# Kernel tuning notes

Hardware: AMD Instinct MI355X
Metric: run time of the kernel (lower is better)

The kernel has to match this reference:

```python
import jax, jax.numpy as jnp
import numpy as np

B, S, D = 2, 2048, 1024
H = 16
HD = D // H  # 64
EPS = 1e-5
ROPE_BASE = 10000.0


def _rope_cos_sin(seq_len, head_dim, dtype):
    # inv_freq over even channel indices, standard rotate-half RoPE
    inv_freq = 1.0 / (ROPE_BASE ** (jnp.arange(0, head_dim, 2, dtype=jnp.float32) / head_dim))
    ang = jnp.arange(seq_len, dtype=jnp.float32)[:, None] * inv_freq[None, :]  # [S, HD/2]
    emb = jnp.concatenate([ang, ang], axis=-1)  # [S, HD]
    return jnp.cos(emb).astype(dtype), jnp.sin(emb).astype(dtype)


def _rotate_half(x):
    x1, x2 = jnp.split(x, 2, axis=-1)
    return jnp.concatenate([-x2, x1], axis=-1)


def setup_inputs() -> dict:
    key = jax.random.key(0)
    ks = jax.random.split(key, 5)
    std = 0.023  # default init_method: normal(mean=0, std=0.023)
    return {
        "hidden_states": jax.random.normal(ks[0], (B, S, D), dtype=jnp.float32),
        "ln_gamma": jnp.ones((D,), dtype=jnp.float32),
        "ln_beta": jnp.zeros((D,), dtype=jnp.float32),
        "qkv_weight": jax.random.normal(ks[1], (3 * D, D), dtype=jnp.float32) * std,
        "qkv_bias": jax.random.normal(ks[2], (3 * D,), dtype=jnp.float32) * std,
        "proj_weight": jax.random.normal(ks[3], (D, D), dtype=jnp.float32) * std,
        "proj_bias": jax.random.normal(ks[4], (D,), dtype=jnp.float32) * std,
    }


def reference(hidden_states, ln_gamma, ln_beta, qkv_weight, qkv_bias, proj_weight, proj_bias):
    b, s, d = hidden_states.shape
    # --- input LayerNorm ---
    mu = jnp.mean(hidden_states, axis=-1, keepdims=True)
    var = jnp.mean(jnp.square(hidden_states - mu), axis=-1, keepdims=True)
    x = (hidden_states - mu) * jax.lax.rsqrt(var + EPS) * ln_gamma + ln_beta

    # --- fused QKV projection (interleaved per-head q,k,v) ---
    qkv = x @ qkv_weight.T + qkv_bias  # [B,S,3D]
    qkv = qkv.reshape(b, s, H, 3, HD)
    q, k, v = qkv[..., 0, :], qkv[..., 1, :], qkv[..., 2, :]  # each [B,S,H,HD]

    # --- RoPE on q and k ---
    cos, sin = _rope_cos_sin(s, HD, q.dtype)  # [S,HD]
    cos = cos[None, :, None, :]
    sin = sin[None, :, None, :]
    q = q * cos + _rotate_half(q) * sin
    k = k * cos + _rotate_half(k) * sin

    # --- causal scaled-dot-product attention ---
    scale = 1.0 / jnp.sqrt(jnp.asarray(HD, dtype=q.dtype))
    scores = jnp.einsum("bqhd,bkhd->bhqk", q, k) * scale  # [B,H,S,S]
    causal = jnp.tril(jnp.ones((s, s), dtype=bool))
    scores = jnp.where(causal[None, None, :, :], scores, jnp.finfo(scores.dtype).min)
    probs = jax.nn.softmax(scores, axis=-1)
    ctx = jnp.einsum("bhqk,bkhd->bqhd", probs, v).reshape(b, s, d)

    # --- output projection ---
    return ctx @ proj_weight.T + proj_bias
```

## Files before the change

kernel.cpp:

```cpp
#include <hip/hip_runtime.h>
#include <math.h>

#define B_  2
#define S_  2048
#define D_  1024
#define H_  16
#define HD_ 64
#define BS_ (B_ * S_)

typedef __bf16 bf16_t;
typedef __bf16 bf16x8 __attribute__((ext_vector_type(8)));
typedef __bf16 bf16x4 __attribute__((ext_vector_type(4)));
typedef float  f32x4  __attribute__((ext_vector_type(4)));
typedef short  s16x4  __attribute__((ext_vector_type(4)));

#define QSCALE 0.18033688011112042f
#define FREQC  0.28782313662425575f

__device__ __forceinline__ void async_ld16(const bf16_t* g, bf16_t* l)
{
    __builtin_amdgcn_global_load_lds(
        (const __attribute__((address_space(1))) void*)g,
        (__attribute__((address_space(3))) void*)l,
        16, 0, 0);
}

__device__ __forceinline__ int chunk_base(int t)
{
    if (t < 8)  return t;
    if (t < 16) return 8 + 2 * (t - 8);
    if (t < 24) return 24 + 3 * (t - 16);
    return 48 + 4 * (t - 24);
}

__global__ __launch_bounds__(256) void ln_cvt(const float* __restrict__ x,
                                              const float* __restrict__ gamma,
                                              const float* __restrict__ beta,
                                              bf16_t* __restrict__ y,
                                              const float* __restrict__ wa,
                                              const float* __restrict__ wb,
                                              bf16_t* __restrict__ oa,
                                              bf16_t* __restrict__ ob)
{
    if (blockIdx.x >= BS_) {
        int idx = (blockIdx.x - BS_) * 256 + threadIdx.x;
        const int NA = 3 * D_ * D_ / 4;
        if (idx < NA) {
            float4 v = ((const float4*)wa)[idx];
            bf16x4 p;
            p[0] = (bf16_t)v.x; p[1] = (bf16_t)v.y; p[2] = (bf16_t)v.z; p[3] = (bf16_t)v.w;
            ((bf16x4*)oa)[idx] = p;
        } else {
            int j = idx - NA;
            float4 v = ((const float4*)wb)[j];
            bf16x4 p;
            p[0] = (bf16_t)v.x; p[1] = (bf16_t)v.y; p[2] = (bf16_t)v.z; p[3] = (bf16_t)v.w;
            ((bf16x4*)ob)[j] = p;
        }
        return;
    }
    int row = blockIdx.x;
    float4 v = ((const float4*)(x + (size_t)row * D_))[threadIdx.x];
    float sum = v.x + v.y + v.z + v.w;
    float sq  = v.x * v.x + v.y * v.y + v.z * v.z + v.w * v.w;
#pragma unroll
    for (int off = 32; off > 0; off >>= 1) {
        sum += __shfl_down(sum, off);
        sq  += __shfl_down(sq, off);
    }
    __shared__ float s_sum[4], s_sq[4];
    int wave = threadIdx.x >> 6;
    if ((threadIdx.x & 63) == 0) { s_sum[wave] = sum; s_sq[wave] = sq; }
    __syncthreads();
    float tsum = s_sum[0] + s_sum[1] + s_sum[2] + s_sum[3];
    float tsq  = s_sq[0] + s_sq[1] + s_sq[2] + s_sq[3];
    float mean = tsum * (1.0f / D_);
    float var  = tsq * (1.0f / D_) - mean * mean;
    float rstd = rsqrtf(var + 1e-5f);
    float4 g = ((const float4*)gamma)[threadIdx.x];
    float4 b = ((const float4*)beta)[threadIdx.x];
    bf16x4 o;
    o[0] = (bf16_t)((v.x - mean) * rstd * g.x + b.x);
    o[1] = (bf16_t)((v.y - mean) * rstd * g.y + b.y);
    o[2] = (bf16_t)((v.z - mean) * rstd * g.z + b.z);
    o[3] = (bf16_t)((v.w - mean) * rstd * g.w + b.w);
    *(bf16x4*)&y[(size_t)row * D_ + threadIdx.x * 4] = o;
}

template<int MODE, int TM>
__global__ __launch_bounds__(256) void gemm_bf16(const bf16_t* __restrict__ A,
                                                 const bf16_t* __restrict__ W,
                                                 const float* __restrict__ bias,
                                                 float* __restrict__ outf,
                                                 bf16_t* __restrict__ qout,
                                                 bf16_t* __restrict__ kout,
                                                 bf16_t* __restrict__ vout,
                                                 int M, int N, int K)
{
    constexpr int ASZ = TM * 32;
    constexpr int BUF = ASZ + 4096;
    constexpr int SMEM = (MODE == 1) ? 18432 : 2 * BUF;
    constexpr int MI = (TM == 128) ? 4 : 2;
    __shared__ bf16_t smem[SMEM];
    const int bm = blockIdx.y * TM, bn = blockIdx.x * 128;
    const int tid = threadIdx.x;
    const int wave = tid >> 6, lane = tid & 63;
    const int ln16 = lane & 15, quad = lane >> 4;
    const int wr = (wave >> 1) * (TM / 2), wc = (wave & 1) * 64;
    const int slot_a = (quad ^ (ln16 & 3)) * 8;

    f32x4 acc[MI][4];
#pragma unroll
    for (int i = 0; i < MI; i++)
#pragma unroll
        for (int j = 0; j < 4; j++) acc[i][j] = (f32x4){0.f, 0.f, 0.f, 0.f};

#pragma unroll
    for (int j = 0; j < TM / 64; j++) {
        int e = j * 256 + tid;
        int r = e >> 2, cg = ((e & 3) ^ (r & 3)) * 8;
        async_ld16(&A[(size_t)(bm + r) * K + cg], smem + e * 8);
    }
#pragma unroll
    for (int j = 0; j < 2; j++) {
        int e = j * 256 + tid;
        int r = e >> 2, cg = ((e & 3) ^ (r & 3)) * 8;
        async_ld16(&W[(size_t)(bn + r) * K + cg], smem + ASZ + e * 8);
    }
    __syncthreads();

    for (int k0 = 0, it = 0; k0 < K; k0 += 32, it++) {
        const bf16_t* cur = smem + (it & 1) * BUF;
        bf16_t* nxt = smem + ((it & 1) ^ 1) * BUF;
        if (k0 + 32 < K) {
#pragma unroll
            for (int j = 0; j < TM / 64; j++) {
                int e = j * 256 + tid;
                int r = e >> 2, cg = ((e & 3) ^ (r & 3)) * 8;
                async_ld16(&A[(size_t)(bm + r) * K + k0 + 32 + cg], nxt + e * 8);
            }
#pragma unroll
            for (int j = 0; j < 2; j++) {
                int e = j * 256 + tid;
                int r = e >> 2, cg = ((e & 3) ^ (r & 3)) * 8;
                async_ld16(&W[(size_t)(bn + r) * K + k0 + 32 + cg], nxt + ASZ + e * 8);
            }
        }

        bf16x8 af[MI], bf[4];
#pragma unroll
        for (int mi = 0; mi < MI; mi++)
            af[mi] = *(const bf16x8*)&cur[(wr + mi * 16 + ln16) * 32 + slot_a];
#pragma unroll
        for (int ni = 0; ni < 4; ni++)
            bf[ni] = *(const bf16x8*)&cur[ASZ + (wc + ni * 16 + ln16) * 32 + slot_a];
#pragma unroll
        for (int mi = 0; mi < MI; mi++)
#pragma unroll
            for (int ni = 0; ni < 4; ni++)
                acc[mi][ni] = __builtin_amdgcn_mfma_f32_16x16x32_bf16(
                    af[mi], bf[ni], acc[mi][ni], 0, 0, 0);

        __syncthreads();
    }

#pragma unroll
    for (int ni = 0; ni < 4; ni++) {
        float bb = bias[bn + wc + ni * 16 + ln16];
#pragma unroll
        for (int mi = 0; mi < MI; mi++)
#pragma unroll
            for (int r = 0; r < 4; r++) acc[mi][ni][r] += bb;
    }

    if (MODE == 0) {
#pragma unroll
        for (int ni = 0; ni < 4; ni++) {
            int n = bn + wc + ni * 16 + ln16;
#pragma unroll
            for (int mi = 0; mi < MI; mi++)
#pragma unroll
                for (int r = 0; r < 4; r++)
                    outf[(size_t)(bm + wr + mi * 16 + quad * 4 + r) * N + n] = acc[mi][ni][r];
        }
    } else {
        const int n64 = (bn + wc) >> 6;
        const int t = n64 % 3, h = n64 / 3;
        bf16_t* T = smem + wave * (64 * 72);
        if (t == 2) {
#pragma unroll
            for (int mi = 0; mi < 4; mi++) {
#pragma unroll
                for (int ni = 0; ni < 4; ni++) {
                    bf16x4 pk;
#pragma unroll
                    for (int r = 0; r < 4; r++) pk[r] = (bf16_t)acc[mi][ni][r];
                    *(bf16x4*)&T[(ni * 16 + ln16) * 72 + mi * 16 + quad * 4] = pk;
                }
            }
            int m0 = bm + wr;
            int bi = m0 >> 11, s0g = m0 & (S_ - 1);
#pragma unroll
            for (int e = lane; e < 512; e += 64) {
                int hd_l = e >> 3, c8 = (e & 7) << 3;
                *(bf16x8*)&vout[((size_t)(bi * H_ + h) * HD_ + hd_l) * S_ + s0g + c8] =
                    *(const bf16x8*)&T[hd_l * 72 + c8];
            }
        } else {
            float fr0 = __expf(-(float)ln16 * FREQC);
            float fr1 = __expf(-(float)(16 + ln16) * FREQC);
            float sc = (t == 0) ? QSCALE : 1.0f;
#pragma unroll
            for (int mi = 0; mi < 4; mi++) {
#pragma unroll
                for (int r = 0; r < 4; r++) {
                    int m = bm + wr + mi * 16 + quad * 4 + r;
                    float s = (float)(m & (S_ - 1));
                    float sn0, cs0, sn1, cs1;
                    __sincosf(s * fr0, &sn0, &cs0);
                    __sincosf(s * fr1, &sn1, &cs1);
                    int rowo = (mi * 16 + quad * 4 + r) * 72;
                    float x1 = acc[mi][0][r], x2 = acc[mi][2][r];
                    T[rowo + ln16]      = (bf16_t)((x1 * cs0 - x2 * sn0) * sc);
                    T[rowo + 32 + ln16] = (bf16_t)((x2 * cs0 + x1 * sn0) * sc);
                    x1 = acc[mi][1][r]; x2 = acc[mi][3][r];
                    T[rowo + 16 + ln16] = (bf16_t)((x1 * cs1 - x2 * sn1) * sc);
                    T[rowo + 48 + ln16] = (bf16_t)((x2 * cs1 + x1 * sn1) * sc);
                }
            }
            bf16_t* dst = (t == 0) ? qout : kout;
#pragma unroll
            for (int e = lane; e < 512; e += 64) {
                int row_l = e >> 3, c8 = (e & 7) << 3;
                int m = bm + wr + row_l;
                int b = m >> 11, s = m & (S_ - 1);
                *(bf16x8*)&dst[((size_t)(b * H_ + h) * S_ + s) * HD_ + c8] =
                    *(const bf16x8*)&T[row_l * 72 + c8];
            }
        }
    }
}

__global__ __launch_bounds__(512) void attn_p1(const bf16_t* __restrict__ q_buf,
                                               const bf16_t* __restrict__ k_buf,
                                               const bf16_t* __restrict__ v_t,
                                               bf16_t* __restrict__ part_o,
                                               float* __restrict__ part_l)
{
    __shared__ bf16_t KS[2][4096];
    __shared__ bf16_t VS[2][4096];

    const int h = blockIdx.y, b = blockIdx.z;
    const int xx = 39 - blockIdx.x;
    int T, c;
    if (xx < 4)       { T = xx;                 c = 0; }
    else if (xx < 12) { int y = xx - 4;  T = 4 + (y >> 1); c = y & 1; }
    else if (xx < 24) { int y = xx - 12; int q = y / 3; T = 8 + q; c = y - 3 * q; }
    else              { int y = xx - 24; T = 12 + (y >> 2); c = y & 3; }
    const int k0c = c * 8;
    const int k1c = min(2 * T + 1, k0c + 7);

    const int tid = threadIdx.x;
    const int wave = tid >> 6, lane = tid & 63;
    const int ln16 = lane & 15, quad = lane >> 4;
    const int w0 = T * 128 + wave * 16;
    const int dt = w0 >> 6;
    const int s7 = ln16 & 7;

    const bf16_t* qb = q_buf + (size_t)(b * H_ + h) * S_ * HD_;
    const bf16_t* kb = k_buf + (size_t)(b * H_ + h) * S_ * HD_;
    const bf16_t* vb = v_t  + (size_t)(b * H_ + h) * HD_ * S_;

    const int r0 = tid >> 3, c0 = ((tid & 7) ^ (r0 & 7)) * 8;

    bf16x8 qf[2];
#pragma unroll
    for (int kc = 0; kc < 2; kc++)
        qf[kc] = *(const bf16x8*)&qb[(size_t)(w0 + ln16) * HD_ + kc * 32 + quad * 8];

    f32x4 o[4];
#pragma unroll
    for (int mi = 0; mi < 4; mi++) o[mi] = (f32x4){0.f, 0.f, 0.f, 0.f};
    float l_i = 0.f;

    async_ld16(&kb[(size_t)(k0c * 64 + r0) * HD_ + c0], &KS[0][tid * 8]);
    async_ld16(&vb[(size_t)r0 * S_ + k0c * 64 + c0], &VS[0][tid * 8]);
    __syncthreads();

    for (int kt = k0c; kt <= k1c; kt++) {
        const int cb = (kt - k0c) & 1;
        if (kt < k1c) {
            const int nb = cb ^ 1, kn = kt + 1;
            async_ld16(&kb[(size_t)(kn * 64 + r0) * HD_ + c0], &KS[nb][tid * 8]);
            async_ld16(&vb[(size_t)r0 * S_ + kn * 64 + c0], &VS[nb][tid * 8]);
        }

        const bf16_t* Kc = &KS[cb][0];
        const bf16_t* Vc = &VS[cb][0];

        f32x4 st[4];
#pragma unroll
        for (int cbx = 0; cbx < 4; cbx++) st[cbx] = (f32x4){0.f, 0.f, 0.f, 0.f};
#pragma unroll
        for (int kc = 0; kc < 2; kc++)
#pragma unroll
            for (int cbx = 0; cbx < 4; cbx++) {
                bf16x8 kf = *(const bf16x8*)&Kc[(cbx * 16 + ln16) * 64 + ((kc * 4 + quad) ^ s7) * 8];
                st[cbx] = __builtin_amdgcn_mfma_f32_16x16x32_bf16(kf, qf[kc], st[cbx], 0, 0, 0);
            }

        if (kt >= dt) {
            int q_g = w0 + ln16;
#pragma unroll
            for (int cbx = 0; cbx < 4; cbx++) {
                int key0 = kt * 64 + cbx * 16 + quad * 4;
#pragma unroll
                for (int r = 0; r < 4; r++)
                    if (key0 + r > q_g) st[cbx][r] = -1e30f;
            }
        }

#pragma unroll
        for (int cbx = 0; cbx < 4; cbx++)
#pragma unroll
            for (int r = 0; r < 4; r++) {
                float p = exp2f(st[cbx][r]);
                st[cbx][r] = p;
                l_i += p;
            }

        s16x4 pf4[4];
#pragma unroll
        for (int cbx = 0; cbx < 4; cbx++) {
            union { bf16x4 hv; s16x4 sv; } u;
#pragma unroll
            for (int r = 0; r < 4; r++) u.hv[r] = (bf16_t)st[cbx][r];
            pf4[cbx] = u.sv;
        }

#pragma unroll
        for (int cbx = 0; cbx < 4; cbx++) {
            int slot = ((cbx * 2 + (quad >> 1)) ^ s7) * 8 + (quad & 1) * 4;
#pragma unroll
            for (int mi = 0; mi < 4; mi++) {
                union { bf16x4 hv; s16x4 sv; } uv;
                uv.hv = *(const bf16x4*)&Vc[(mi * 16 + ln16) * 64 + slot];
                o[mi] = __builtin_amdgcn_mfma_f32_16x16x16bf16_1k(uv.sv, pf4[cbx], o[mi], 0, 0, 0);
            }
        }

        __syncthreads();
    }

    l_i += __shfl_xor(l_i, 16);
    l_i += __shfl_xor(l_i, 32);

    const int t_tile = dt;
    const size_t pidx = (size_t)(b * H_ + h) * 80 + chunk_base(t_tile) + c;
    bf16_t* po = part_o + pidx * 4096;
    const int q_l = (wave & 3) * 16 + ln16;
#pragma unroll
    for (int mi = 0; mi < 4; mi++) {
        bf16x4 pk;
#pragma unroll
        for (int r = 0; r < 4; r++) pk[r] = (bf16_t)o[mi][r];
        *(bf16x4*)&po[q_l * 64 + mi * 16 + quad * 4] = pk;
    }
    if (quad == 0)
        part_l[pidx * 64 + q_l] = l_i;
}

__global__ __launch_bounds__(256) void attn_p2(const bf16_t* __restrict__ part_o,
                                               const float* __restrict__ part_l,
                                               bf16_t* __restrict__ ctx)
{
    const int t = blockIdx.x, h = blockIdx.y, b = blockIdx.z;
    const int nch = (t >> 3) + 1;
    const size_t p0 = (size_t)(b * H_ + h) * 80 + chunk_base(t);
    const int q_l = threadIdx.x >> 2;
    const int hg = (threadIdx.x & 3) * 16;

    float L = 0.f;
    float f0[8] = {0,0,0,0,0,0,0,0}, f1[8] = {0,0,0,0,0,0,0,0};
#pragma unroll
    for (int i = 0; i < 4; i++) {
        if (i < nch) {
            L += part_l[(p0 + i) * 64 + q_l];
            const bf16_t* oi = part_o + (p0 + i) * 4096 + q_l * 64 + hg;
            bf16x8 v0 = *(const bf16x8*)oi;
            bf16x8 v1 = *(const bf16x8*)(oi + 8);
#pragma unroll
            for (int j = 0; j < 8; j++) {
                f0[j] += (float)v0[j];
                f1[j] += (float)v1[j];
            }
        }
    }
    float invL = 1.0f / L;
    bf16x8 out0, out1;
#pragma unroll
    for (int j = 0; j < 8; j++) {
        out0[j] = (bf16_t)(f0[j] * invL);
        out1[j] = (bf16_t)(f1[j] * invL);
    }
    bf16_t* dst = &ctx[(size_t)(b * S_ + t * 64 + q_l) * D_ + h * HD_ + hg];
    *(bf16x8*)dst = out0;
    *(bf16x8*)(dst + 8) = out1;
}

extern "C" void kernel_launch(void* const* d_in, const int* in_sizes, int n_in,
                              void* d_out, int out_size, void* d_ws, size_t ws_size,
                              hipStream_t stream)
{
    const float* hidden = (const float*)d_in[0];
    const float* gamma  = (const float*)d_in[1];
    const float* beta   = (const float*)d_in[2];
    const float* qkv_w  = (const float*)d_in[3];
    const float* qkv_b  = (const float*)d_in[4];
    const float* proj_w = (const float*)d_in[5];
    const float* proj_b = (const float*)d_in[6];
    float* out = (float*)d_out;

    char* ws = (char*)d_ws;
    const size_t MB = 1024 * 1024;
    bf16_t* x_ln = (bf16_t*)(ws);
    bf16_t* wq   = (bf16_t*)(ws +  8 * MB);
    bf16_t* wp   = (bf16_t*)(ws + 14 * MB);
    bf16_t* qbf  = (bf16_t*)(ws + 16 * MB);
    bf16_t* kbf  = (bf16_t*)(ws + 24 * MB);
    bf16_t* vtb  = (bf16_t*)(ws + 32 * MB);
    bf16_t* ctx  = (bf16_t*)(ws + 40 * MB);
    bf16_t* po   = (bf16_t*)(ws + 48 * MB);
    float*  pl   = (float*)(ws + 68 * MB);

    ln_cvt<<<BS_ + 4096, 256, 0, stream>>>(hidden, gamma, beta, x_ln,
                                           qkv_w, proj_w, wq, wp);
    gemm_bf16<1, 128><<<dim3(24, 32), 256, 0, stream>>>(
        x_ln, wq, qkv_b, nullptr, qbf, kbf, vtb, BS_, 3 * D_, D_);
    attn_p1<<<dim3(40, H_, B_), 512, 0, stream>>>(qbf, kbf, vtb, po, pl);
    attn_p2<<<dim3(32, H_, B_), 256, 0, stream>>>(po, pl, ctx);
    gemm_bf16<0, 64><<<dim3(8, 64), 256, 0, stream>>>(
        ctx, wp, proj_b, out, nullptr, nullptr, nullptr, BS_, D_, D_);
}
```

Baseline: 186.6 us.

## Skip fully-masked key tiles and compute row sums via MFMA with ones

Inside the attention loop, waves now skip QK/PV compute for key tiles beyond their diagonal tile, and masking runs only on the diagonal tile. The softmax denominator is now accumulated by an extra MFMA against a ones vector using the bf16 probabilities, replacing scalar adds and cross-lane shuffles. Probability packing uses a packed bf16 conversion builtin when one is available. This trims VALU work and wasted MFMAs on causal tiles, but the row sum is now taken from bf16-rounded values and adds one MFMA per block of 16 keys.

```diff
diff --git a/kernel.cpp b/kernel.cpp
--- a/kernel.cpp
+++ b/kernel.cpp
@@ -23,6 +23,23 @@
         (const __attribute__((address_space(1))) void*)g,
         (__attribute__((address_space(3))) void*)l,
         16, 0, 0);
+}
+
+__device__ __forceinline__ s16x4 pack_bf16x4(float a, float b, float c, float d)
+{
+#if __has_builtin(__builtin_amdgcn_cvt_pk_bf16_f32)
+    typedef __bf16 bf16x2_t __attribute__((ext_vector_type(2)));
+    bf16x2_t lo = __builtin_amdgcn_cvt_pk_bf16_f32(a, b);
+    bf16x2_t hi = __builtin_amdgcn_cvt_pk_bf16_f32(c, d);
+    union { struct { bf16x2_t l, h; } p; s16x4 sv; } u;
+    u.p.l = lo; u.p.h = hi;
+    return u.sv;
+#else
+    union { bf16x4 hv; s16x4 sv; } u;
+    u.hv[0] = (bf16_t)a; u.hv[1] = (bf16_t)b;
+    u.hv[2] = (bf16_t)c; u.hv[3] = (bf16_t)d;
+    return u.sv;
+#endif
 }
 
 __device__ __forceinline__ int chunk_base(int t)
@@ -281,7 +298,12 @@
     f32x4 o[4];
 #pragma unroll
     for (int mi = 0; mi < 4; mi++) o[mi] = (f32x4){0.f, 0.f, 0.f, 0.f};
-    float l_i = 0.f;
+    f32x4 ol = (f32x4){0.f, 0.f, 0.f, 0.f};
+
+    union { bf16x4 hv; s16x4 sv; } ones_u;
+    ones_u.hv[0] = (bf16_t)1.0f; ones_u.hv[1] = (bf16_t)1.0f;
+    ones_u.hv[2] = (bf16_t)1.0f; ones_u.hv[3] = (bf16_t)1.0f;
+    const s16x4 ones = ones_u.sv;
 
     async_ld16(&kb[(size_t)(k0c * 64 + r0) * HD_ + c0], &KS[0][tid * 8]);
     async_ld16(&vb[(size_t)r0 * S_ + k0c * 64 + c0], &VS[0][tid * 8]);
@@ -295,68 +317,59 @@
             async_ld16(&vb[(size_t)r0 * S_ + kn * 64 + c0], &VS[nb][tid * 8]);
         }
 
-        const bf16_t* Kc = &KS[cb][0];
-        const bf16_t* Vc = &VS[cb][0];
-
-        f32x4 st[4];
-#pragma unroll
-        for (int cbx = 0; cbx < 4; cbx++) st[cbx] = (f32x4){0.f, 0.f, 0.f, 0.f};
-#pragma unroll
-        for (int kc = 0; kc < 2; kc++)
+        if (kt <= dt) {
+            const bf16_t* Kc = &KS[cb][0];
+            const bf16_t* Vc = &VS[cb][0];
+
+            f32x4 st[4];
+#pragma unroll
+            for (int cbx = 0; cbx < 4; cbx++) st[cbx] = (f32x4){0.f, 0.f, 0.f, 0.f};
+#pragma unroll
+            for (int kc = 0; kc < 2; kc++)
+#pragma unroll
+                for (int cbx = 0; cbx < 4; cbx++) {
+                    bf16x8 kf = *(const bf16x8*)&Kc[(cbx * 16 + ln16) * 64 + ((kc * 4 + quad) ^ s7) * 8];
+                    st[cbx] = __builtin_amdgcn_mfma_f32_16x16x32_bf16(kf, qf[kc], st[cbx], 0, 0, 0);
+                }
+
+            if (kt == dt) {
+                int q_g = w0 + ln16;
+#pragma unroll
+                for (int cbx = 0; cbx < 4; cbx++) {
+                    int key0 = kt * 64 + cbx * 16 + quad * 4;
+#pragma unroll
+                    for (int r = 0; r < 4; r++)
+                        if (key0 + r > q_g) st[cbx][r] = -1e30f;
+                }
+            }
+
+            s16x4 pf4[4];
 #pragma unroll
             for (int cbx = 0; cbx < 4; cbx++) {
-                bf16x8 kf = *(const bf16x8*)&Kc[(cbx * 16 + ln16) * 64 + ((kc * 4 + quad) ^ s7) * 8];
-                st[cbx] = __builtin_amdgcn_mfma_f32_16x16x32_bf16(kf, qf[kc], st[cbx], 0, 0, 0);
-            }
-
-        if (kt >= dt) {
-            int q_g = w0 + ln16;
+                float p0 = exp2f(st[cbx][0]);
+                float p1 = exp2f(st[cbx][1]);
+                float p2 = exp2f(st[cbx][2]);
+                float p3 = exp2f(st[cbx][3]);
+                pf4[cbx] = pack_bf16x4(p0, p1, p2, p3);
+            }
+
 #pragma unroll
             for (int cbx = 0; cbx < 4; cbx++) {
-                int key0 = kt * 64 + cbx * 16 + quad * 4;
-#pragma unroll
-                for (int r = 0; r < 4; r++)
-                    if (key0 + r > q_g) st[cbx][r] = -1e30f;
-            }
-        }
-
-#pragma unroll
-        for (int cbx = 0; cbx < 4; cbx++)
-#pragma unroll
-            for (int r = 0; r < 4; r++) {
-                float p = exp2f(st[cbx][r]);
-                st[cbx][r] = p;
-                l_i += p;
-            }
-
-        s16x4 pf4[4];
-#pragma unroll
-        for (int cbx = 0; cbx < 4; cbx++) {
-            union { bf16x4 hv; s16x4 sv; } u;
-#pragma unroll
-            for (int r = 0; r < 4; r++) u.hv[r] = (bf16_t)st[cbx][r];
-            pf4[cbx] = u.sv;
-        }
-
-#pragma unroll
-        for (int cbx = 0; cbx < 4; cbx++) {
-            int slot = ((cbx * 2 + (quad >> 1)) ^ s7) * 8 + (quad & 1) * 4;
-#pragma unroll
-            for (int mi = 0; mi < 4; mi++) {
-                union { bf16x4 hv; s16x4 sv; } uv;
-                uv.hv = *(const bf16x4*)&Vc[(mi * 16 + ln16) * 64 + slot];
-                o[mi] = __builtin_amdgcn_mfma_f32_16x16x16bf16_1k(uv.sv, pf4[cbx], o[mi], 0, 0, 0);
+                int slot = ((cbx * 2 + (quad >> 1)) ^ s7) * 8 + (quad & 1) * 4;
+#pragma unroll
+                for (int mi = 0; mi < 4; mi++) {
+                    union { bf16x4 hv; s16x4 sv; } uv;
+                    uv.hv = *(const bf16x4*)&Vc[(mi * 16 + ln16) * 64 + slot];
+                    o[mi] = __builtin_amdgcn_mfma_f32_16x16x16bf16_1k(uv.sv, pf4[cbx], o[mi], 0, 0, 0);
+                }
+                ol = __builtin_amdgcn_mfma_f32_16x16x16bf16_1k(ones, pf4[cbx], ol, 0, 0, 0);
             }
         }
 
         __syncthreads();
     }
 
-    l_i += __shfl_xor(l_i, 16);
-    l_i += __shfl_xor(l_i, 32);
-
-    const int t_tile = dt;
-    const size_t pidx = (size_t)(b * H_ + h) * 80 + chunk_base(t_tile) + c;
+    const size_t pidx = (size_t)(b * H_ + h) * 80 + chunk_base(dt) + c;
     bf16_t* po = part_o + pidx * 4096;
     const int q_l = (wave & 3) * 16 + ln16;
 #pragma unroll
@@ -367,7 +380,7 @@
         *(bf16x4*)&po[q_l * 64 + mi * 16 + quad * 4] = pk;
     }
     if (quad == 0)
-        part_l[pidx * 64 + q_l] = l_i;
+        part_l[pidx * 64 + q_l] = ol[0];
 }
 
 __global__ __launch_bounds__(256) void attn_p2(const bf16_t* __restrict__ part_o,
```

Result: no change. 188.3 us (+0.9%).
